# Kernel tuning notes

Measured on AMD Instinct MI355X. Metric: run time of the kernel, lower is better.

Reference implementation:

```python
import jax, jax.numpy as jnp
import numpy as np

B, S, D, H, HID = 64, 1024, 128, 4, 512
HD = D // H  # head dim = 32
EPS = 1e-5


def layer_norm(x, gamma, beta):
    mu = jnp.mean(x, axis=-1, keepdims=True)
    var = jnp.mean(jnp.square(x - mu), axis=-1, keepdims=True)
    return (x - mu) * jax.lax.rsqrt(var + EPS) * gamma + beta


def setup_inputs() -> dict:
    key = jax.random.key(0)
    ks = jax.random.split(key, 16)
    w = lambda k, shp: (jax.random.normal(k, shp, dtype=jnp.float32) * 0.02)
    return {
        "seq": jax.random.normal(ks[0], (B, S, D), dtype=jnp.float32),
        "mask": jnp.ones((B, S, 1), dtype=jnp.float32),
        "Wq": w(ks[1], (D, D)), "bq": jnp.zeros((D,), jnp.float32),
        "Wk": w(ks[2], (D, D)), "bk": jnp.zeros((D,), jnp.float32),
        "Wv": w(ks[3], (D, D)), "bv": jnp.zeros((D,), jnp.float32),
        "g1": jnp.ones((D,), jnp.float32), "be1": jnp.zeros((D,), jnp.float32),
        "g2": jnp.ones((D,), jnp.float32), "be2": jnp.zeros((D,), jnp.float32),
        "W1": w(ks[4], (D, HID)), "bm1": jnp.zeros((HID,), jnp.float32),
        "W2": w(ks[5], (HID, D)), "bm2": jnp.zeros((D,), jnp.float32),
    }


def reference(seq, mask, Wq, bq, Wk, bk, Wv, bv, g1, be1, g2, be2, W1, bm1, W2, bm2):
    # pre-norm queries; keys/values come from the RAW seq (SASRec quirk)
    q_in = layer_norm(seq, g1, be1)           # [B,S,D]
    keys = seq

    Q = (q_in @ Wq + bq).reshape(B, S, H, HD)
    K = (keys @ Wk + bk).reshape(B, S, H, HD)
    V = (keys @ Wv + bv).reshape(B, S, H, HD)

    scores = jnp.einsum("bqhd,bkhd->bhqk", Q, K) / jnp.sqrt(jnp.float32(HD))

    # key padding mask from sign of abs-sum over feature dim
    key_mask = jnp.sign(jnp.sum(jnp.abs(keys), axis=-1))      # [B,S]
    scores = jnp.where(key_mask[:, None, None, :] == 0, -jnp.inf, scores)

    # causal mask
    causal = jnp.tril(jnp.ones((S, S), dtype=bool))
    scores = jnp.where(causal[None, None], scores, -jnp.inf)

    w = jax.nn.softmax(scores, axis=-1)
    w = jnp.nan_to_num(w, nan=0.0, posinf=0.0, neginf=0.0)

    # query padding mask (on the NORMALIZED queries)
    query_mask = jnp.sign(jnp.sum(jnp.abs(q_in), axis=-1))    # [B,S]
    w = w * query_mask[:, None, :, None]
    attentions = w                                            # [B,H,S,S]

    attn_out = jnp.einsum("bhqk,bkhd->bqhd", w, V).reshape(B, S, D)

    x = attn_out + q_in
    x = layer_norm(x, g2, be2)
    h = jax.nn.relu(x @ W1 + bm1)
    y = h @ W2 + bm2 + x
    y = y * mask
    return y, attentions
```

## Files before the change

### kernel.cpp

```cpp
#include <hip/hip_runtime.h>
#include <cstddef>
#include <cstdint>

#define BB 64
#define SS 1024
#define DDIM 128
#define NH 4
#define HDIM 32
#define HIDD 512
#define EPSF 1e-5f
#define SCALEF 0.17677669529663687f
#define LOG2E 1.4426950408889634f

typedef __attribute__((ext_vector_type(8))) short short8;
typedef __attribute__((ext_vector_type(4))) short short4_t;
typedef __attribute__((ext_vector_type(4))) float f32x4;
typedef unsigned short ushort_t;

__device__ __forceinline__ unsigned short f2bf(float f) {
  unsigned u = __builtin_bit_cast(unsigned, f);
  unsigned r = (u + 0x7FFFu + ((u >> 16) & 1u)) >> 16;
  return (unsigned short)r;
}
__device__ __forceinline__ float bf2f(ushort_t h) {
  unsigned u = ((unsigned)h) << 16;
  return __builtin_bit_cast(float, u);
}

__global__ __launch_bounds__(256) void k_cvtw(
    const float* __restrict__ Wq, const float* __restrict__ Wk,
    const float* __restrict__ Wv, const float* __restrict__ W1,
    const float* __restrict__ W2,
    ushort_t* __restrict__ WqT, ushort_t* __restrict__ WkT,
    ushort_t* __restrict__ WvT, ushort_t* __restrict__ W1T,
    ushort_t* __restrict__ W2T) {
  __shared__ float tile[32][33];
  const int bid = blockIdx.x;
  const float* src; ushort_t* dst; int K, N, t0;
  if (bid < 16)       { src = Wq; dst = WqT; K = 128; N = 128; t0 = bid; }
  else if (bid < 32)  { src = Wk; dst = WkT; K = 128; N = 128; t0 = bid - 16; }
  else if (bid < 48)  { src = Wv; dst = WvT; K = 128; N = 128; t0 = bid - 32; }
  else if (bid < 112) { src = W1; dst = W1T; K = 128; N = 512; t0 = bid - 48; }
  else                { src = W2; dst = W2T; K = 512; N = 128; t0 = bid - 112; }
  const int ntile = N >> 5;
  const int k0 = (t0 / ntile) * 32, n0 = (t0 % ntile) * 32;
  const int t = threadIdx.x;
  const int r = t >> 3, c = (t & 7) * 4;
  float4 v = *(const float4*)(src + (size_t)(k0 + r) * N + n0 + c);
  tile[r][c] = v.x; tile[r][c + 1] = v.y; tile[r][c + 2] = v.z; tile[r][c + 3] = v.w;
  __syncthreads();
  ushort4 o;
  o.x = f2bf(tile[c + 0][r]); o.y = f2bf(tile[c + 1][r]);
  o.z = f2bf(tile[c + 2][r]); o.w = f2bf(tile[c + 3][r]);
  *(ushort4*)(dst + (size_t)(n0 + r) * K + k0 + c) = o;
}

__global__ __launch_bounds__(256) void k_ln1(const float* __restrict__ seq,
    const float* __restrict__ g1, const float* __restrict__ be1,
    ushort_t* __restrict__ q_in16, ushort_t* __restrict__ seq16,
    float* __restrict__ qmask, float* __restrict__ kmask) {
  const int t = threadIdx.x;
  const int r = t >> 5, cl = (t & 31) * 4;
  const int row = blockIdx.x * 8 + r;
  const size_t base = (size_t)row * DDIM + cl;
  const f32x4 v4 = *(const f32x4*)(seq + base);
  float sum = v4[0] + v4[1] + v4[2] + v4[3];
  float asum = fabsf(v4[0]) + fabsf(v4[1]) + fabsf(v4[2]) + fabsf(v4[3]);
  #pragma unroll
  for (int o = 1; o < 32; o <<= 1) { sum += __shfl_xor(sum, o); asum += __shfl_xor(asum, o); }
  const float mean = sum * (1.f / DDIM);
  f32x4 d;
  #pragma unroll
  for (int j = 0; j < 4; ++j) d[j] = v4[j] - mean;
  float sq = d[0] * d[0] + d[1] * d[1] + d[2] * d[2] + d[3] * d[3];
  #pragma unroll
  for (int o = 1; o < 32; o <<= 1) sq += __shfl_xor(sq, o);
  const float rsq = rsqrtf(sq * (1.f / DDIM) + EPSF);
  const float4 g4 = *(const float4*)(g1 + cl);
  const float4 b4 = *(const float4*)(be1 + cl);
  float qv[4];
  qv[0] = d[0] * rsq * g4.x + b4.x; qv[1] = d[1] * rsq * g4.y + b4.y;
  qv[2] = d[2] * rsq * g4.z + b4.z; qv[3] = d[3] * rsq * g4.w + b4.w;
  short4_t q4, s4;
  #pragma unroll
  for (int j = 0; j < 4; ++j) { q4[j] = (short)f2bf(qv[j]); s4[j] = (short)f2bf(v4[j]); }
  *(short4_t*)(q_in16 + base) = q4;
  *(short4_t*)(seq16 + base) = s4;
  float aq = fabsf(qv[0]) + fabsf(qv[1]) + fabsf(qv[2]) + fabsf(qv[3]);
  #pragma unroll
  for (int o = 1; o < 32; o <<= 1) aq += __shfl_xor(aq, o);
  if ((t & 31) == 0) {
    kmask[row] = asum > 0.f ? 1.f : 0.f;
    qmask[row] = aq > 0.f ? 1.f : 0.f;
  }
}

__global__ __launch_bounds__(256) void k_qkv_mfma(
    const ushort_t* __restrict__ q_in16, const ushort_t* __restrict__ seq16,
    const ushort_t* __restrict__ WqT, const ushort_t* __restrict__ WkT,
    const ushort_t* __restrict__ WvT,
    const float* __restrict__ bq, const float* __restrict__ bk,
    const float* __restrict__ bv,
    ushort_t* __restrict__ Qo, ushort_t* __restrict__ Ko,
    ushort_t* __restrict__ Vo) {
  const int m = blockIdx.y;
  const int t = threadIdx.x, w = t >> 6, lane = t & 63;
  const int lr = lane & 15, lg = lane >> 4;
  const int row = blockIdx.x * 64 + w * 16;

  if (m == 0) {
    const float sc = SCALEF * LOG2E;
    short8 a[4];
    #pragma unroll
    for (int s = 0; s < 4; ++s)
      a[s] = *(const short8*)(q_in16 + (size_t)(row + lr) * DDIM + s * 32 + lg * 8);
    #pragma unroll
    for (int nt = 0; nt < 8; ++nt) {
      f32x4 acc = {0.f, 0.f, 0.f, 0.f};
      #pragma unroll
      for (int s = 0; s < 4; ++s) {
        short8 b = *(const short8*)(WqT + (size_t)(nt * 16 + lr) * DDIM + s * 32 + lg * 8);
        acc = __builtin_amdgcn_mfma_f32_16x16x32_bf16(b, a[s], acc, 0, 0, 0);
      }
      const int n0 = nt * 16 + lg * 4;
      const float4 bb4 = *(const float4*)(bq + n0);
      short4_t o4;
      o4[0] = (short)f2bf((acc[0] + bb4.x) * sc);
      o4[1] = (short)f2bf((acc[1] + bb4.y) * sc);
      o4[2] = (short)f2bf((acc[2] + bb4.z) * sc);
      o4[3] = (short)f2bf((acc[3] + bb4.w) * sc);
      *(short4_t*)(Qo + (size_t)(row + lr) * DDIM + n0) = o4;
    }
  } else {
    short8 a[4];
    #pragma unroll
    for (int s = 0; s < 4; ++s)
      a[s] = *(const short8*)(seq16 + (size_t)(row + lr) * DDIM + s * 32 + lg * 8);
    #pragma unroll
    for (int nt = 0; nt < 8; ++nt) {
      f32x4 accK = {0.f, 0.f, 0.f, 0.f}, accV = {0.f, 0.f, 0.f, 0.f};
      #pragma unroll
      for (int s = 0; s < 4; ++s) {
        short8 bk8 = *(const short8*)(WkT + (size_t)(nt * 16 + lr) * DDIM + s * 32 + lg * 8);
        short8 bv8 = *(const short8*)(WvT + (size_t)(nt * 16 + lr) * DDIM + s * 32 + lg * 8);
        accK = __builtin_amdgcn_mfma_f32_16x16x32_bf16(bk8, a[s], accK, 0, 0, 0);
        accV = __builtin_amdgcn_mfma_f32_16x16x32_bf16(bv8, a[s], accV, 0, 0, 0);
      }
      const int n0 = nt * 16 + lg * 4;
      const float4 bk4 = *(const float4*)(bk + n0);
      const float4 bv4 = *(const float4*)(bv + n0);
      short4_t k4, v4;
      k4[0] = (short)f2bf(accK[0] + bk4.x); v4[0] = (short)f2bf(accV[0] + bv4.x);
      k4[1] = (short)f2bf(accK[1] + bk4.y); v4[1] = (short)f2bf(accV[1] + bv4.y);
      k4[2] = (short)f2bf(accK[2] + bk4.z); v4[2] = (short)f2bf(accV[2] + bv4.z);
      k4[3] = (short)f2bf(accK[3] + bk4.w); v4[3] = (short)f2bf(accV[3] + bv4.w);
      *(short4_t*)(Ko + (size_t)(row + lr) * DDIM + n0) = k4;
      *(short4_t*)(Vo + (size_t)(row + lr) * DDIM + n0) = v4;
    }
  }
}

__global__ __launch_bounds__(256) void k_attn_mfma(
    const ushort_t* __restrict__ Q, const ushort_t* __restrict__ K,
    const ushort_t* __restrict__ V,
    const float* __restrict__ qmask, const float* __restrict__ kmask,
    float* __restrict__ attn, float* __restrict__ xo) {
  __shared__ __align__(16) ushort_t Ks[2][64 * 40];
  __shared__ __align__(16) ushort_t Vts[2][32 * 72];
  __shared__ __align__(16) ushort_t Wb[4][16 * 88];

  const int t = threadIdx.x;
  const int w = t >> 6, lane = t & 63, lr = lane & 15, lg = lane >> 4;
  const int qi = 15 - (int)blockIdx.x;
  const int q0 = qi << 6;
  const int h = blockIdx.y, b = blockIdx.z;
  const int kend = q0 + 64;
  const int nch = kend >> 6;

  const size_t bS = (size_t)b * SS;
  const ushort_t* Qh = Q + bS * DDIM + h * HDIM;
  const ushort_t* Kh = K + bS * DDIM + h * HDIM;
  const ushort_t* Vh = V + bS * DDIM + h * HDIM;
  float* attn_bh = attn + (size_t)(b * NH + h) * ((size_t)SS * SS);

  {
    const int cnt4 = (SS - kend) >> 2;
    const f32x4 z = {0.f, 0.f, 0.f, 0.f};
    for (int r = w; r < 64; r += 4) {
      float* rowp = attn_bh + (size_t)(q0 + r) * SS + kend;
      for (int c = lane; c < cnt4; c += 64)
        __builtin_nontemporal_store(z, (f32x4*)(rowp + (size_t)c * 4));
    }
  }

  const int qrow = q0 + w * 16 + lr;
  const short8 qf = *(const short8*)(Qh + (size_t)qrow * DDIM + lg * 8);

  const int skr = t >> 2, skc = (t & 3) * 8;

  float lsum = 0.f;
  {
    short8 kreg = *(const short8*)(Kh + (size_t)skr * DDIM + skc);
    *(short8*)(Ks[0] + skr * 40 + skc) = kreg;
    __syncthreads();
    for (int c = 0; c < nch; ++c) {
      const int kc = c << 6;
      const int cur = c & 1;
      if (c + 1 < nch)
        kreg = *(const short8*)(Kh + (size_t)(kc + 64 + skr) * DDIM + skc);
      short8 kf[4];
      #pragma unroll
      for (int T = 0; T < 4; ++T)
        kf[T] = *(const short8*)(Ks[cur] + (T * 16 + lr) * 40 + lg * 8);
      f32x4 acc[4];
      #pragma unroll
      for (int T = 0; T < 4; ++T)
        acc[T] = __builtin_amdgcn_mfma_f32_16x16x32_bf16(kf[T], qf,
                                                         (f32x4){0.f, 0.f, 0.f, 0.f}, 0, 0, 0);
      #pragma unroll
      for (int T = 0; T < 4; ++T) {
        const int k0 = kc + T * 16 + lg * 4;
        const float4 km4 = *(const float4*)(kmask + bS + k0);
        #pragma unroll
        for (int r = 0; r < 4; ++r) {
          const float kmv = r == 0 ? km4.x : (r == 1 ? km4.y : (r == 2 ? km4.z : km4.w));
          const bool dead = (kmv == 0.f) || (k0 + r > qrow);
          lsum += dead ? 0.f : exp2f(acc[T][r]);
        }
      }
      if (c + 1 < nch)
        *(short8*)(Ks[cur ^ 1] + skr * 40 + skc) = kreg;
      __syncthreads();
    }
  }
  float ssum = lsum;
  ssum += __shfl_xor(ssum, 16);
  ssum += __shfl_xor(ssum, 32);
  const float qm = qmask[bS + qrow];
  const float inv = (ssum > 0.f) ? qm / ssum : 0.f;

  ushort_t* myW = &Wb[w][0];
  f32x4 o0 = {0.f, 0.f, 0.f, 0.f}, o1 = {0.f, 0.f, 0.f, 0.f};

  {
    short8 kreg = *(const short8*)(Kh + (size_t)skr * DDIM + skc);
    short8 vreg = *(const short8*)(Vh + (size_t)lane * DDIM + w * 8);
    *(short8*)(Ks[0] + skr * 40 + skc) = kreg;
    #pragma unroll
    for (int j = 0; j < 8; ++j) Vts[0][(w * 8 + j) * 72 + lane] = (ushort_t)vreg[j];
    __syncthreads();
    for (int c = 0; c < nch; ++c) {
      const int kc = c << 6;
      const int cur = c & 1;
      if (c + 1 < nch) {
        kreg = *(const short8*)(Kh + (size_t)(kc + 64 + skr) * DDIM + skc);
        vreg = *(const short8*)(Vh + (size_t)(kc + 64 + lane) * DDIM + w * 8);
      }
      short8 kf[4];
      #pragma unroll
      for (int T = 0; T < 4; ++T)
        kf[T] = *(const short8*)(Ks[cur] + (T * 16 + lr) * 40 + lg * 8);
      f32x4 acc[4];
      #pragma unroll
      for (int T = 0; T < 4; ++T)
        acc[T] = __builtin_amdgcn_mfma_f32_16x16x32_bf16(kf[T], qf,
                                                         (f32x4){0.f, 0.f, 0.f, 0.f}, 0, 0, 0);
      #pragma unroll
      for (int T = 0; T < 4; ++T) {
        const int k0 = kc + T * 16 + lg * 4;
        const float4 km4 = *(const float4*)(kmask + bS + k0);
        f32x4 wv4;
        #pragma unroll
        for (int r = 0; r < 4; ++r) {
          const float kmv = r == 0 ? km4.x : (r == 1 ? km4.y : (r == 2 ? km4.z : km4.w));
          const bool dead = (kmv == 0.f) || (k0 + r > qrow);
          wv4[r] = dead ? 0.f : exp2f(acc[T][r]) * inv;
        }
        __builtin_nontemporal_store(wv4, (f32x4*)(attn_bh + (size_t)qrow * SS + k0));
        short4_t p4;
        p4[0] = (short)f2bf(wv4[0]); p4[1] = (short)f2bf(wv4[1]);
        p4[2] = (short)f2bf(wv4[2]); p4[3] = (short)f2bf(wv4[3]);
        *(short4_t*)(myW + lr * 88 + T * 16 + lg * 4) = p4;
      }
      const short8 af0 = *(const short8*)(myW + lr * 88 + lg * 8);
      const short8 af1 = *(const short8*)(myW + lr * 88 + 32 + lg * 8);
      const short8 vb00 = *(const short8*)(Vts[cur] + (size_t)(lr) * 72 + lg * 8);
      const short8 vb10 = *(const short8*)(Vts[cur] + (size_t)(lr) * 72 + 32 + lg * 8);
      const short8 vb01 = *(const short8*)(Vts[cur] + (size_t)(16 + lr) * 72 + lg * 8);
      const short8 vb11 = *(const short8*)(Vts[cur] + (size_t)(16 + lr) * 72 + 32 + lg * 8);
      o0 = __builtin_amdgcn_mfma_f32_16x16x32_bf16(vb00, af0, o0, 0, 0, 0);
      o0 = __builtin_amdgcn_mfma_f32_16x16x32_bf16(vb10, af1, o0, 0, 0, 0);
      o1 = __builtin_amdgcn_mfma_f32_16x16x32_bf16(vb01, af0, o1, 0, 0, 0);
      o1 = __builtin_amdgcn_mfma_f32_16x16x32_bf16(vb11, af1, o1, 0, 0, 0);
      if (c + 1 < nch) {
        *(short8*)(Ks[cur ^ 1] + skr * 40 + skc) = kreg;
        #pragma unroll
        for (int j = 0; j < 8; ++j) Vts[cur ^ 1][(w * 8 + j) * 72 + lane] = (ushort_t)vreg[j];
      }
      __syncthreads();
    }
  }

  {
    float* op = xo + (bS + qrow) * DDIM + h * HDIM;
    *(f32x4*)(op + lg * 4) = o0;
    *(f32x4*)(op + 16 + lg * 4) = o1;
  }
}

__global__ __launch_bounds__(256) void k_mlp_fused(
    const float* __restrict__ xo, const ushort_t* __restrict__ q_in16,
    const float* __restrict__ g2, const float* __restrict__ be2,
    const ushort_t* __restrict__ W1T, const float* __restrict__ bm1,
    const ushort_t* __restrict__ W2T, const float* __restrict__ bm2,
    const float* __restrict__ mask, float* __restrict__ y) {
  __shared__ __align__(16) ushort_t xls[64 * 136];
  __shared__ __align__(16) ushort_t hs[4][16 * 140];
  const int t = threadIdx.x, w = t >> 6, lane = t & 63;
  const int lr = lane & 15, lg = lane >> 4;
  const int row0 = blockIdx.x * 64;

  {
    const int r = t >> 2, s = t & 3;
    const size_t base = (size_t)(row0 + r) * DDIM + s * 32;
    float v[32];
    float sum = 0.f, sq = 0.f;
    #pragma unroll
    for (int i = 0; i < 4; ++i) {
      const f32x4 x4a = *(const f32x4*)(xo + base + i * 8);
      const f32x4 x4b = *(const f32x4*)(xo + base + i * 8 + 4);
      const short8 q8 = *(const short8*)(q_in16 + base + i * 8);
      #pragma unroll
      for (int j = 0; j < 4; ++j) {
        v[i * 8 + j] = x4a[j] + bf2f((ushort_t)q8[j]);
        v[i * 8 + 4 + j] = x4b[j] + bf2f((ushort_t)q8[4 + j]);
      }
    }
    #pragma unroll
    for (int i = 0; i < 32; ++i) { sum += v[i]; sq += v[i] * v[i]; }
    sum += __shfl_xor(sum, 1); sum += __shfl_xor(sum, 2);
    sq  += __shfl_xor(sq, 1);  sq  += __shfl_xor(sq, 2);
    const float mean = sum * (1.f / DDIM);
    const float var = sq * (1.f / DDIM) - mean * mean;
    const float rsq = rsqrtf(var + EPSF);
    #pragma unroll
    for (int i = 0; i < 8; ++i) {
      const f32x4 g4 = *(const f32x4*)(g2 + s * 32 + i * 4);
      const f32x4 b4 = *(const f32x4*)(be2 + s * 32 + i * 4);
      short4_t o4;
      #pragma unroll
      for (int j = 0; j < 4; ++j)
        o4[j] = (short)f2bf((v[i * 4 + j] - mean) * rsq * g4[j] + b4[j]);
      *(short4_t*)(xls + r * 136 + s * 32 + i * 4) = o4;
    }
  }
  __syncthreads();

  ushort_t* myh = &hs[w][0];
  short8 xa[4];
  #pragma unroll
  for (int s = 0; s < 4; ++s)
    xa[s] = *(const short8*)(xls + (w * 16 + lr) * 136 + s * 32 + lg * 8);

  f32x4 yacc[8];
  #pragma unroll
  for (int i = 0; i < 8; ++i) yacc[i] = (f32x4){0.f, 0.f, 0.f, 0.f};

  for (int c = 0; c < 4; ++c) {
    #pragma unroll
    for (int nt = 0; nt < 8; ++nt) {
      f32x4 acc = {0.f, 0.f, 0.f, 0.f};
      #pragma unroll
      for (int s = 0; s < 4; ++s) {
        short8 b = *(const short8*)(W1T + (size_t)(c * 128 + nt * 16 + lr) * DDIM + s * 32 + lg * 8);
        acc = __builtin_amdgcn_mfma_f32_16x16x32_bf16(b, xa[s], acc, 0, 0, 0);
      }
      const int n0 = nt * 16 + lg * 4;
      const float4 bb4 = *(const float4*)(bm1 + c * 128 + n0);
      short4_t hp;
      hp[0] = (short)f2bf(fmaxf(acc[0] + bb4.x, 0.f));
      hp[1] = (short)f2bf(fmaxf(acc[1] + bb4.y, 0.f));
      hp[2] = (short)f2bf(fmaxf(acc[2] + bb4.z, 0.f));
      hp[3] = (short)f2bf(fmaxf(acc[3] + bb4.w, 0.f));
      *(short4_t*)(myh + lr * 140 + n0) = hp;
    }
    short8 a2[4];
    #pragma unroll
    for (int s = 0; s < 4; ++s)
      a2[s] = *(const short8*)(myh + lr * 140 + s * 32 + lg * 8);
    #pragma unroll
    for (int nt = 0; nt < 8; ++nt) {
      #pragma unroll
      for (int s = 0; s < 4; ++s) {
        short8 b = *(const short8*)(W2T + (size_t)(nt * 16 + lr) * HIDD + c * 128 + s * 32 + lg * 8);
        yacc[nt] = __builtin_amdgcn_mfma_f32_16x16x32_bf16(b, a2[s], yacc[nt], 0, 0, 0);
      }
    }
  }

  const int rr = row0 + w * 16 + lr;
  const float mk = mask[rr];
  #pragma unroll
  for (int nt = 0; nt < 8; ++nt) {
    const int n0 = nt * 16 + lg * 4;
    const float4 bb4 = *(const float4*)(bm2 + n0);
    const ushort4 xv = *(const ushort4*)(xls + (w * 16 + lr) * 136 + n0);
    f32x4 out;
    out[0] = (yacc[nt][0] + bb4.x + bf2f(xv.x)) * mk;
    out[1] = (yacc[nt][1] + bb4.y + bf2f(xv.y)) * mk;
    out[2] = (yacc[nt][2] + bb4.z + bf2f(xv.z)) * mk;
    out[3] = (yacc[nt][3] + bb4.w + bf2f(xv.w)) * mk;
    *(f32x4*)(y + (size_t)rr * DDIM + n0) = out;
  }
}

extern "C" void kernel_launch(void* const* d_in, const int* in_sizes, int n_in,
                              void* d_out, int out_size, void* d_ws, size_t ws_size,
                              hipStream_t stream) {
  const float* seq  = (const float*)d_in[0];
  const float* mask = (const float*)d_in[1];
  const float* Wq = (const float*)d_in[2];
  const float* bq = (const float*)d_in[3];
  const float* Wk = (const float*)d_in[4];
  const float* bk = (const float*)d_in[5];
  const float* Wv = (const float*)d_in[6];
  const float* bv = (const float*)d_in[7];
  const float* g1 = (const float*)d_in[8];
  const float* be1 = (const float*)d_in[9];
  const float* g2 = (const float*)d_in[10];
  const float* be2 = (const float*)d_in[11];
  const float* W1 = (const float*)d_in[12];
  const float* bm1 = (const float*)d_in[13];
  const float* W2 = (const float*)d_in[14];
  const float* bm2 = (const float*)d_in[15];

  float* ws   = (float*)d_ws;
  float* xb   = ws;
  float* qmk  = ws + 8388608;
  float* kmk  = ws + 8454144;
  ushort_t* sbase  = (ushort_t*)(ws + 8519680);
  ushort_t* Qb     = sbase;
  ushort_t* Kb     = sbase + 8388608;
  ushort_t* Vb     = sbase + 16777216;
  ushort_t* q_in16 = sbase + 25165824;
  ushort_t* seq16  = sbase + 33554432;
  ushort_t* WqT    = sbase + 41943040;
  ushort_t* WkT    = WqT + 16384;
  ushort_t* WvT    = WkT + 16384;
  ushort_t* W1T    = WvT + 16384;
  ushort_t* W2T    = W1T + 65536;

  float* y    = (float*)d_out;
  float* attn = y + 8388608;

  hipLaunchKernelGGL(k_cvtw, dim3(176), dim3(256), 0, stream,
                     Wq, Wk, Wv, W1, W2, WqT, WkT, WvT, W1T, W2T);
  hipLaunchKernelGGL(k_ln1, dim3(BB * SS / 8), dim3(256), 0, stream,
                     seq, g1, be1, q_in16, seq16, qmk, kmk);
  hipLaunchKernelGGL(k_qkv_mfma, dim3(1024, 2), dim3(256), 0, stream,
                     q_in16, seq16, WqT, WkT, WvT, bq, bk, bv, Qb, Kb, Vb);
  hipLaunchKernelGGL(k_attn_mfma, dim3(16, NH, BB), dim3(256), 0, stream,
                     Qb, Kb, Vb, qmk, kmk, attn, xb);
  hipLaunchKernelGGL(k_mlp_fused, dim3(1024), dim3(256), 0, stream,
                     xb, q_in16, g2, be2, W1T, bm1, W2T, bm2, mask, y);
}
```

Measured before the change: 573.7 us.

## Fuse LayerNorm into QKV projection and give attention blocks 128 query rows

```diff
diff --git a/kernel.cpp b/kernel.cpp
--- a/kernel.cpp
+++ b/kernel.cpp
@@ -55,112 +55,120 @@
   *(ushort4*)(dst + (size_t)(n0 + r) * K + k0 + c) = o;
 }
 
-__global__ __launch_bounds__(256) void k_ln1(const float* __restrict__ seq,
+__global__ __launch_bounds__(256) void k_ln1_qkv(
+    const float* __restrict__ seq,
     const float* __restrict__ g1, const float* __restrict__ be1,
-    ushort_t* __restrict__ q_in16, ushort_t* __restrict__ seq16,
-    float* __restrict__ qmask, float* __restrict__ kmask) {
-  const int t = threadIdx.x;
-  const int r = t >> 5, cl = (t & 31) * 4;
-  const int row = blockIdx.x * 8 + r;
-  const size_t base = (size_t)row * DDIM + cl;
-  const f32x4 v4 = *(const f32x4*)(seq + base);
-  float sum = v4[0] + v4[1] + v4[2] + v4[3];
-  float asum = fabsf(v4[0]) + fabsf(v4[1]) + fabsf(v4[2]) + fabsf(v4[3]);
-  #pragma unroll
-  for (int o = 1; o < 32; o <<= 1) { sum += __shfl_xor(sum, o); asum += __shfl_xor(asum, o); }
-  const float mean = sum * (1.f / DDIM);
-  f32x4 d;
-  #pragma unroll
-  for (int j = 0; j < 4; ++j) d[j] = v4[j] - mean;
-  float sq = d[0] * d[0] + d[1] * d[1] + d[2] * d[2] + d[3] * d[3];
-  #pragma unroll
-  for (int o = 1; o < 32; o <<= 1) sq += __shfl_xor(sq, o);
-  const float rsq = rsqrtf(sq * (1.f / DDIM) + EPSF);
-  const float4 g4 = *(const float4*)(g1 + cl);
-  const float4 b4 = *(const float4*)(be1 + cl);
-  float qv[4];
-  qv[0] = d[0] * rsq * g4.x + b4.x; qv[1] = d[1] * rsq * g4.y + b4.y;
-  qv[2] = d[2] * rsq * g4.z + b4.z; qv[3] = d[3] * rsq * g4.w + b4.w;
-  short4_t q4, s4;
-  #pragma unroll
-  for (int j = 0; j < 4; ++j) { q4[j] = (short)f2bf(qv[j]); s4[j] = (short)f2bf(v4[j]); }
-  *(short4_t*)(q_in16 + base) = q4;
-  *(short4_t*)(seq16 + base) = s4;
-  float aq = fabsf(qv[0]) + fabsf(qv[1]) + fabsf(qv[2]) + fabsf(qv[3]);
-  #pragma unroll
-  for (int o = 1; o < 32; o <<= 1) aq += __shfl_xor(aq, o);
-  if ((t & 31) == 0) {
-    kmask[row] = asum > 0.f ? 1.f : 0.f;
-    qmask[row] = aq > 0.f ? 1.f : 0.f;
-  }
-}
-
-__global__ __launch_bounds__(256) void k_qkv_mfma(
-    const ushort_t* __restrict__ q_in16, const ushort_t* __restrict__ seq16,
     const ushort_t* __restrict__ WqT, const ushort_t* __restrict__ WkT,
     const ushort_t* __restrict__ WvT,
     const float* __restrict__ bq, const float* __restrict__ bk,
     const float* __restrict__ bv,
+    ushort_t* __restrict__ q_in16,
     ushort_t* __restrict__ Qo, ushort_t* __restrict__ Ko,
-    ushort_t* __restrict__ Vo) {
-  const int m = blockIdx.y;
-  const int t = threadIdx.x, w = t >> 6, lane = t & 63;
+    ushort_t* __restrict__ Vo,
+    float* __restrict__ qmask, float* __restrict__ kmask) {
+  __shared__ __align__(16) ushort_t qls[64 * 136];
+  __shared__ __align__(16) ushort_t sls[64 * 136];
+  const int t = threadIdx.x;
+  const int row0 = blockIdx.x * 64;
+
+  {
+    const int r = t >> 2, s = t & 3;
+    const size_t base = (size_t)(row0 + r) * DDIM + s * 32;
+    float v[32];
+    float sum = 0.f, asum = 0.f;
+    #pragma unroll
+    for (int i = 0; i < 8; ++i) {
+      const f32x4 x4 = *(const f32x4*)(seq + base + i * 4);
+      #pragma unroll
+      for (int j = 0; j < 4; ++j) {
+        v[i * 4 + j] = x4[j];
+        sum += x4[j]; asum += fabsf(x4[j]);
+      }
+    }
+    sum += __shfl_xor(sum, 1); sum += __shfl_xor(sum, 2);
+    asum += __shfl_xor(asum, 1); asum += __shfl_xor(asum, 2);
+    const float mean = sum * (1.f / DDIM);
+    float sq = 0.f;
+    #pragma unroll
+    for (int i = 0; i < 32; ++i) { const float d = v[i] - mean; sq += d * d; }
+    sq += __shfl_xor(sq, 1); sq += __shfl_xor(sq, 2);
+    const float rsq = rsqrtf(sq * (1.f / DDIM) + EPSF);
+    float aq = 0.f;
+    #pragma unroll
+    for (int i = 0; i < 8; ++i) {
+      const f32x4 g4 = *(const f32x4*)(g1 + s * 32 + i * 4);
+      const f32x4 b4 = *(const f32x4*)(be1 + s * 32 + i * 4);
+      short4_t q4, s4v;
+      #pragma unroll
+      for (int j = 0; j < 4; ++j) {
+        const float qv = (v[i * 4 + j] - mean) * rsq * g4[j] + b4[j];
+        aq += fabsf(qv);
+        q4[j] = (short)f2bf(qv);
+        s4v[j] = (short)f2bf(v[i * 4 + j]);
+      }
+      *(short4_t*)(qls + r * 136 + s * 32 + i * 4) = q4;
+      *(short4_t*)(sls + r * 136 + s * 32 + i * 4) = s4v;
+      *(short4_t*)(q_in16 + base + i * 4) = q4;
+    }
+    aq += __shfl_xor(aq, 1); aq += __shfl_xor(aq, 2);
+    if (s == 0) {
+      kmask[row0 + r] = asum > 0.f ? 1.f : 0.f;
+      qmask[row0 + r] = aq > 0.f ? 1.f : 0.f;
+    }
+  }
+  __syncthreads();
+
+  const int w = t >> 6, lane = t & 63;
   const int lr = lane & 15, lg = lane >> 4;
-  const int row = blockIdx.x * 64 + w * 16;
-
-  if (m == 0) {
-    const float sc = SCALEF * LOG2E;
-    short8 a[4];
-    #pragma unroll
-    for (int s = 0; s < 4; ++s)
-      a[s] = *(const short8*)(q_in16 + (size_t)(row + lr) * DDIM + s * 32 + lg * 8);
-    #pragma unroll
-    for (int nt = 0; nt < 8; ++nt) {
-      f32x4 acc = {0.f, 0.f, 0.f, 0.f};
-      #pragma unroll
-      for (int s = 0; s < 4; ++s) {
-        short8 b = *(const short8*)(WqT + (size_t)(nt * 16 + lr) * DDIM + s * 32 + lg * 8);
-        acc = __builtin_amdgcn_mfma_f32_16x16x32_bf16(b, a[s], acc, 0, 0, 0);
-      }
-      const int n0 = nt * 16 + lg * 4;
-      const float4 bb4 = *(const float4*)(bq + n0);
-      short4_t o4;
-      o4[0] = (short)f2bf((acc[0] + bb4.x) * sc);
-      o4[1] = (short)f2bf((acc[1] + bb4.y) * sc);
-      o4[2] = (short)f2bf((acc[2] + bb4.z) * sc);
-      o4[3] = (short)f2bf((acc[3] + bb4.w) * sc);
-      *(short4_t*)(Qo + (size_t)(row + lr) * DDIM + n0) = o4;
-    }
-  } else {
-    short8 a[4];
-    #pragma unroll
-    for (int s = 0; s < 4; ++s)
-      a[s] = *(const short8*)(seq16 + (size_t)(row + lr) * DDIM + s * 32 + lg * 8);
-    #pragma unroll
-    for (int nt = 0; nt < 8; ++nt) {
-      f32x4 accK = {0.f, 0.f, 0.f, 0.f}, accV = {0.f, 0.f, 0.f, 0.f};
-      #pragma unroll
-      for (int s = 0; s < 4; ++s) {
-        short8 bk8 = *(const short8*)(WkT + (size_t)(nt * 16 + lr) * DDIM + s * 32 + lg * 8);
-        short8 bv8 = *(const short8*)(WvT + (size_t)(nt * 16 + lr) * DDIM + s * 32 + lg * 8);
-        accK = __builtin_amdgcn_mfma_f32_16x16x32_bf16(bk8, a[s], accK, 0, 0, 0);
-        accV = __builtin_amdgcn_mfma_f32_16x16x32_bf16(bv8, a[s], accV, 0, 0, 0);
-      }
-      const int n0 = nt * 16 + lg * 4;
-      const float4 bk4 = *(const float4*)(bk + n0);
-      const float4 bv4 = *(const float4*)(bv + n0);
-      short4_t k4, v4;
-      k4[0] = (short)f2bf(accK[0] + bk4.x); v4[0] = (short)f2bf(accV[0] + bv4.x);
-      k4[1] = (short)f2bf(accK[1] + bk4.y); v4[1] = (short)f2bf(accV[1] + bv4.y);
-      k4[2] = (short)f2bf(accK[2] + bk4.z); v4[2] = (short)f2bf(accV[2] + bv4.z);
-      k4[3] = (short)f2bf(accK[3] + bk4.w); v4[3] = (short)f2bf(accV[3] + bv4.w);
-      *(short4_t*)(Ko + (size_t)(row + lr) * DDIM + n0) = k4;
-      *(short4_t*)(Vo + (size_t)(row + lr) * DDIM + n0) = v4;
-    }
-  }
-}
-
-__global__ __launch_bounds__(256) void k_attn_mfma(
+  const int rloc = w * 16 + lr;
+  short8 qa[4], sa[4];
+  #pragma unroll
+  for (int s4 = 0; s4 < 4; ++s4) {
+    qa[s4] = *(const short8*)(qls + rloc * 136 + s4 * 32 + lg * 8);
+    sa[s4] = *(const short8*)(sls + rloc * 136 + s4 * 32 + lg * 8);
+  }
+  const float qsc = SCALEF * LOG2E;
+  #pragma unroll
+  for (int nt = 0; nt < 8; ++nt) {
+    f32x4 acc = {0.f, 0.f, 0.f, 0.f};
+    #pragma unroll
+    for (int s4 = 0; s4 < 4; ++s4) {
+      short8 b = *(const short8*)(WqT + (size_t)(nt * 16 + lr) * DDIM + s4 * 32 + lg * 8);
+      acc = __builtin_amdgcn_mfma_f32_16x16x32_bf16(b, qa[s4], acc, 0, 0, 0);
+    }
+    const int n0 = nt * 16 + lg * 4;
+    const float4 bb4 = *(const float4*)(bq + n0);
+    short4_t o4;
+    o4[0] = (short)f2bf((acc[0] + bb4.x) * qsc);
+    o4[1] = (short)f2bf((acc[1] + bb4.y) * qsc);
+    o4[2] = (short)f2bf((acc[2] + bb4.z) * qsc);
+    o4[3] = (short)f2bf((acc[3] + bb4.w) * qsc);
+    *(short4_t*)(Qo + (size_t)(row0 + rloc) * DDIM + n0) = o4;
+  }
+  #pragma unroll
+  for (int nt = 0; nt < 8; ++nt) {
+    f32x4 accK = {0.f, 0.f, 0.f, 0.f}, accV = {0.f, 0.f, 0.f, 0.f};
+    #pragma unroll
+    for (int s4 = 0; s4 < 4; ++s4) {
+      short8 bk8 = *(const short8*)(WkT + (size_t)(nt * 16 + lr) * DDIM + s4 * 32 + lg * 8);
+      short8 bv8 = *(const short8*)(WvT + (size_t)(nt * 16 + lr) * DDIM + s4 * 32 + lg * 8);
+      accK = __builtin_amdgcn_mfma_f32_16x16x32_bf16(bk8, sa[s4], accK, 0, 0, 0);
+      accV = __builtin_amdgcn_mfma_f32_16x16x32_bf16(bv8, sa[s4], accV, 0, 0, 0);
+    }
+    const int n0 = nt * 16 + lg * 4;
+    const float4 bk4 = *(const float4*)(bk + n0);
+    const float4 bv4 = *(const float4*)(bv + n0);
+    short4_t k4, v4;
+    k4[0] = (short)f2bf(accK[0] + bk4.x); v4[0] = (short)f2bf(accV[0] + bv4.x);
+    k4[1] = (short)f2bf(accK[1] + bk4.y); v4[1] = (short)f2bf(accV[1] + bv4.y);
+    k4[2] = (short)f2bf(accK[2] + bk4.z); v4[2] = (short)f2bf(accV[2] + bv4.z);
+    k4[3] = (short)f2bf(accK[3] + bk4.w); v4[3] = (short)f2bf(accV[3] + bv4.w);
+    *(short4_t*)(Ko + (size_t)(row0 + rloc) * DDIM + n0) = k4;
+    *(short4_t*)(Vo + (size_t)(row0 + rloc) * DDIM + n0) = v4;
+  }
+}
+
+__global__ __launch_bounds__(256, 4) void k_attn_mfma(
     const ushort_t* __restrict__ Q, const ushort_t* __restrict__ K,
     const ushort_t* __restrict__ V,
     const float* __restrict__ qmask, const float* __restrict__ kmask,
@@ -171,10 +179,10 @@
 
   const int t = threadIdx.x;
   const int w = t >> 6, lane = t & 63, lr = lane & 15, lg = lane >> 4;
-  const int qi = 15 - (int)blockIdx.x;
-  const int q0 = qi << 6;
+  const int qi = 7 - (int)blockIdx.x;
+  const int q0 = qi << 7;
   const int h = blockIdx.y, b = blockIdx.z;
-  const int kend = q0 + 64;
+  const int kend = q0 + 128;
   const int nch = kend >> 6;
 
   const size_t bS = (size_t)b * SS;
@@ -186,19 +194,22 @@
   {
     const int cnt4 = (SS - kend) >> 2;
     const f32x4 z = {0.f, 0.f, 0.f, 0.f};
-    for (int r = w; r < 64; r += 4) {
+    for (int r = w; r < 128; r += 4) {
       float* rowp = attn_bh + (size_t)(q0 + r) * SS + kend;
       for (int c = lane; c < cnt4; c += 64)
         __builtin_nontemporal_store(z, (f32x4*)(rowp + (size_t)c * 4));
     }
   }
 
-  const int qrow = q0 + w * 16 + lr;
-  const short8 qf = *(const short8*)(Qh + (size_t)qrow * DDIM + lg * 8);
+  const int qrow0 = q0 + w * 16 + lr;
+  const int qrow1 = qrow0 + 64;
+  const int deadlim = q0 + w * 16 + 15;
+  const short8 qf0 = *(const short8*)(Qh + (size_t)qrow0 * DDIM + lg * 8);
+  const short8 qf1 = *(const short8*)(Qh + (size_t)qrow1 * DDIM + lg * 8);
 
   const int skr = t >> 2, skc = (t & 3) * 8;
 
-  float lsum = 0.f;
+  float lsum0 = 0.f, lsum1 = 0.f;
   {
     short8 kreg = *(const short8*)(Kh + (size_t)skr * DDIM + skc);
     *(short8*)(Ks[0] + skr * 40 + skc) = kreg;
@@ -212,20 +223,42 @@
       #pragma unroll
       for (int T = 0; T < 4; ++T)
         kf[T] = *(const short8*)(Ks[cur] + (T * 16 + lr) * 40 + lg * 8);
-      f32x4 acc[4];
+      float4 km4[4];
       #pragma unroll
       for (int T = 0; T < 4; ++T)
-        acc[T] = __builtin_amdgcn_mfma_f32_16x16x32_bf16(kf[T], qf,
-                                                         (f32x4){0.f, 0.f, 0.f, 0.f}, 0, 0, 0);
-      #pragma unroll
-      for (int T = 0; T < 4; ++T) {
-        const int k0 = kc + T * 16 + lg * 4;
-        const float4 km4 = *(const float4*)(kmask + bS + k0);
-        #pragma unroll
-        for (int r = 0; r < 4; ++r) {
-          const float kmv = r == 0 ? km4.x : (r == 1 ? km4.y : (r == 2 ? km4.z : km4.w));
-          const bool dead = (kmv == 0.f) || (k0 + r > qrow);
-          lsum += dead ? 0.f : exp2f(acc[T][r]);
+        km4[T] = *(const float4*)(kmask + bS + kc + T * 16 + lg * 4);
+      if (kc <= deadlim) {
+        f32x4 acc0[4];
+        #pragma unroll
+        for (int T = 0; T < 4; ++T)
+          acc0[T] = __builtin_amdgcn_mfma_f32_16x16x32_bf16(kf[T], qf0,
+                                                            (f32x4){0.f, 0.f, 0.f, 0.f}, 0, 0, 0);
+        #pragma unroll
+        for (int T = 0; T < 4; ++T) {
+          const int k0 = kc + T * 16 + lg * 4;
+          #pragma unroll
+          for (int r = 0; r < 4; ++r) {
+            const float kmv = r == 0 ? km4[T].x : (r == 1 ? km4[T].y : (r == 2 ? km4[T].z : km4[T].w));
+            const bool dead = (kmv == 0.f) || (k0 + r > qrow0);
+            lsum0 += dead ? 0.f : exp2f(acc0[T][r]);
+          }
+        }
+      }
+      {
+        f32x4 acc1[4];
+        #pragma unroll
+        for (int T = 0; T < 4; ++T)
+          acc1[T] = __builtin_amdgcn_mfma_f32_16x16x32_bf16(kf[T], qf1,
+                                                            (f32x4){0.f, 0.f, 0.f, 0.f}, 0, 0, 0);
+        #pragma unroll
+        for (int T = 0; T < 4; ++T) {
+          const int k0 = kc + T * 16 + lg * 4;
+          #pragma unroll
+          for (int r = 0; r < 4; ++r) {
+            const float kmv = r == 0 ? km4[T].x : (r == 1 ? km4[T].y : (r == 2 ? km4[T].z : km4[T].w));
+            const bool dead = (kmv == 0.f) || (k0 + r > qrow1);
+            lsum1 += dead ? 0.f : exp2f(acc1[T][r]);
+          }
         }
       }
       if (c + 1 < nch)
@@ -233,14 +266,15 @@
       __syncthreads();
     }
   }
-  float ssum = lsum;
-  ssum += __shfl_xor(ssum, 16);
-  ssum += __shfl_xor(ssum, 32);
-  const float qm = qmask[bS + qrow];
-  const float inv = (ssum > 0.f) ? qm / ssum : 0.f;
+  float ssum0 = lsum0, ssum1 = lsum1;
+  ssum0 += __shfl_xor(ssum0, 16); ssum0 += __shfl_xor(ssum0, 32);
+  ssum1 += __shfl_xor(ssum1, 16); ssum1 += __shfl_xor(ssum1, 32);
+  const float inv0 = (ssum0 > 0.f) ? qmask[bS + qrow0] / ssum0 : 0.f;
+  const float inv1 = (ssum1 > 0.f) ? qmask[bS + qrow1] / ssum1 : 0.f;
 
   ushort_t* myW = &Wb[w][0];
   f32x4 o0 = {0.f, 0.f, 0.f, 0.f}, o1 = {0.f, 0.f, 0.f, 0.f};
+  f32x4 o2 = {0.f, 0.f, 0.f, 0.f}, o3 = {0.f, 0.f, 0.f, 0.f};
 
   {
     short8 kreg = *(const short8*)(Kh + (size_t)skr * DDIM + skc);
@@ -260,38 +294,84 @@
       #pragma unroll
       for (int T = 0; T < 4; ++T)
         kf[T] = *(const short8*)(Ks[cur] + (T * 16 + lr) * 40 + lg * 8);
-      f32x4 acc[4];
+      float4 km4[4];
       #pragma unroll
       for (int T = 0; T < 4; ++T)
-        acc[T] = __builtin_amdgcn_mfma_f32_16x16x32_bf16(kf[T], qf,
-                                                         (f32x4){0.f, 0.f, 0.f, 0.f}, 0, 0, 0);
-      #pragma unroll
-      for (int T = 0; T < 4; ++T) {
-        const int k0 = kc + T * 16 + lg * 4;
-        const float4 km4 = *(const float4*)(kmask + bS + k0);
-        f32x4 wv4;
-        #pragma unroll
-        for (int r = 0; r < 4; ++r) {
-          const float kmv = r == 0 ? km4.x : (r == 1 ? km4.y : (r == 2 ? km4.z : km4.w));
-          const bool dead = (kmv == 0.f) || (k0 + r > qrow);
-          wv4[r] = dead ? 0.f : exp2f(acc[T][r]) * inv;
+        km4[T] = *(const float4*)(kmask + bS + kc + T * 16 + lg * 4);
+
+      if (kc <= deadlim) {
+        f32x4 acc0[4];
+        #pragma unroll
+        for (int T = 0; T < 4; ++T)
+          acc0[T] = __builtin_amdgcn_mfma_f32_16x16x32_bf16(kf[T], qf0,
+                                                            (f32x4){0.f, 0.f, 0.f, 0.f}, 0, 0, 0);
+        #pragma unroll
+        for (int T = 0; T < 4; ++T) {
+          const int k0 = kc + T * 16 + lg * 4;
+          f32x4 wv4;
+          #pragma unroll
+          for (int r = 0; r < 4; ++r) {
+            const float kmv = r == 0 ? km4[T].x : (r == 1 ? km4[T].y : (r == 2 ? km4[T].z : km4[T].w));
+            const bool dead = (kmv == 0.f) || (k0 + r > qrow0);
+            wv4[r] = dead ? 0.f : exp2f(acc0[T][r]) * inv0;
+          }
+          __builtin_nontemporal_store(wv4, (f32x4*)(attn_bh + (size_t)qrow0 * SS + k0));
+          short4_t p4;
+          p4[0] = (short)f2bf(wv4[0]); p4[1] = (short)f2bf(wv4[1]);
+          p4[2] = (short)f2bf(wv4[2]); p4[3] = (short)f2bf(wv4[3]);
+          *(short4_t*)(myW + lr * 88 + T * 16 + lg * 4) = p4;
         }
-        __builtin_nontemporal_store(wv4, (f32x4*)(attn_bh + (size_t)qrow * SS + k0));
-        short4_t p4;
-        p4[0] = (short)f2bf(wv4[0]); p4[1] = (short)f2bf(wv4[1]);
-        p4[2] = (short)f2bf(wv4[2]); p4[3] = (short)f2bf(wv4[3]);
-        *(short4_t*)(myW + lr * 88 + T * 16 + lg * 4) = p4;
-      }
-      const short8 af0 = *(const short8*)(myW + lr * 88 + lg * 8);
-      const short8 af1 = *(const short8*)(myW + lr * 88 + 32 + lg * 8);
-      const short8 vb00 = *(const short8*)(Vts[cur] + (size_t)(lr) * 72 + lg * 8);
-      const short8 vb10 = *(const short8*)(Vts[cur] + (size_t)(lr) * 72 + 32 + lg * 8);
-      const short8 vb01 = *(const short8*)(Vts[cur] + (size_t)(16 + lr) * 72 + lg * 8);
-      const short8 vb11 = *(const short8*)(Vts[cur] + (size_t)(16 + lr) * 72 + 32 + lg * 8);
-      o0 = __builtin_amdgcn_mfma_f32_16x16x32_bf16(vb00, af0, o0, 0, 0, 0);
-      o0 = __builtin_amdgcn_mfma_f32_16x16x32_bf16(vb10, af1, o0, 0, 0, 0);
-      o1 = __builtin_amdgcn_mfma_f32_16x16x32_bf16(vb01, af0, o1, 0, 0, 0);
-      o1 = __builtin_amdgcn_mfma_f32_16x16x32_bf16(vb11, af1, o1, 0, 0, 0);
+        const short8 af0 = *(const short8*)(myW + lr * 88 + lg * 8);
+        const short8 af1 = *(const short8*)(myW + lr * 88 + 32 + lg * 8);
+        const short8 vb00 = *(const short8*)(Vts[cur] + (size_t)(lr) * 72 + lg * 8);
+        const short8 vb10 = *(const short8*)(Vts[cur] + (size_t)(lr) * 72 + 32 + lg * 8);
+        const short8 vb01 = *(const short8*)(Vts[cur] + (size_t)(16 + lr) * 72 + lg * 8);
+        const short8 vb11 = *(const short8*)(Vts[cur] + (size_t)(16 + lr) * 72 + 32 + lg * 8);
+        o0 = __builtin_amdgcn_mfma_f32_16x16x32_bf16(vb00, af0, o0, 0, 0, 0);
+        o0 = __builtin_amdgcn_mfma_f32_16x16x32_bf16(vb10, af1, o0, 0, 0, 0);
+        o1 = __builtin_amdgcn_mfma_f32_16x16x32_bf16(vb01, af0, o1, 0, 0, 0);
+        o1 = __builtin_amdgcn_mfma_f32_16x16x32_bf16(vb11, af1, o1, 0, 0, 0);
+      } else {
+        const f32x4 z = {0.f, 0.f, 0.f, 0.f};
+        #pragma unroll
+        for (int T = 0; T < 4; ++T)
+          __builtin_nontemporal_store(z, (f32x4*)(attn_bh + (size_t)qrow0 * SS + kc + T * 16 + lg * 4));
+      }
+
+      {
+        f32x4 acc1[4];
+        #pragma unroll
+        for (int T = 0; T < 4; ++T)
+          acc1[T] = __builtin_amdgcn_mfma_f32_16x16x32_bf16(kf[T], qf1,
+                                                            (f32x4){0.f, 0.f, 0.f, 0.f}, 0, 0, 0);
+        #pragma unroll
+        for (int T = 0; T < 4; ++T) {
+          const int k0 = kc + T * 16 + lg * 4;
+          f32x4 wv4;
+          #pragma unroll
+          for (int r = 0; r < 4; ++r) {
+            const float kmv = r == 0 ? km4[T].x : (r == 1 ? km4[T].y : (r == 2 ? km4[T].z : km4[T].w));
+            const bool dead = (kmv == 0.f) || (k0 + r > qrow1);
+            wv4[r] = dead ? 0.f : exp2f(acc1[T][r]) * inv1;
+          }
+          __builtin_nontemporal_store(wv4, (f32x4*)(attn_bh + (size_t)qrow1 * SS + k0));
+          short4_t p4;
+          p4[0] = (short)f2bf(wv4[0]); p4[1] = (short)f2bf(wv4[1]);
+          p4[2] = (short)f2bf(wv4[2]); p4[3] = (short)f2bf(wv4[3]);
+          *(short4_t*)(myW + lr * 88 + T * 16 + lg * 4) = p4;
+        }
+        const short8 af0 = *(const short8*)(myW + lr * 88 + lg * 8);
+        const short8 af1 = *(const short8*)(myW + lr * 88 + 32 + lg * 8);
+        const short8 vb00 = *(const short8*)(Vts[cur] + (size_t)(lr) * 72 + lg * 8);
+        const short8 vb10 = *(const short8*)(Vts[cur] + (size_t)(lr) * 72 + 32 + lg * 8);
+        const short8 vb01 = *(const short8*)(Vts[cur] + (size_t)(16 + lr) * 72 + lg * 8);
+        const short8 vb11 = *(const short8*)(Vts[cur] + (size_t)(16 + lr) * 72 + 32 + lg * 8);
+        o2 = __builtin_amdgcn_mfma_f32_16x16x32_bf16(vb00, af0, o2, 0, 0, 0);
+        o2 = __builtin_amdgcn_mfma_f32_16x16x32_bf16(vb10, af1, o2, 0, 0, 0);
+        o3 = __builtin_amdgcn_mfma_f32_16x16x32_bf16(vb01, af0, o3, 0, 0, 0);
+        o3 = __builtin_amdgcn_mfma_f32_16x16x32_bf16(vb11, af1, o3, 0, 0, 0);
+      }
+
       if (c + 1 < nch) {
         *(short8*)(Ks[cur ^ 1] + skr * 40 + skc) = kreg;
         #pragma unroll
@@ -302,9 +382,12 @@
   }
 
   {
-    float* op = xo + (bS + qrow) * DDIM + h * HDIM;
-    *(f32x4*)(op + lg * 4) = o0;
-    *(f32x4*)(op + 16 + lg * 4) = o1;
+    float* op0 = xo + (bS + qrow0) * DDIM + h * HDIM;
+    *(f32x4*)(op0 + lg * 4) = o0;
+    *(f32x4*)(op0 + 16 + lg * 4) = o1;
+    float* op1 = xo + (bS + qrow1) * DDIM + h * HDIM;
+    *(f32x4*)(op1 + lg * 4) = o2;
+    *(f32x4*)(op1 + 16 + lg * 4) = o3;
   }
 }
 
@@ -443,8 +526,7 @@
   ushort_t* Kb     = sbase + 8388608;
   ushort_t* Vb     = sbase + 16777216;
   ushort_t* q_in16 = sbase + 25165824;
-  ushort_t* seq16  = sbase + 33554432;
-  ushort_t* WqT    = sbase + 41943040;
+  ushort_t* WqT    = sbase + 33554432;
   ushort_t* WkT    = WqT + 16384;
   ushort_t* WvT    = WkT + 16384;
   ushort_t* W1T    = WvT + 16384;
@@ -455,11 +537,10 @@
 
   hipLaunchKernelGGL(k_cvtw, dim3(176), dim3(256), 0, stream,
                      Wq, Wk, Wv, W1, W2, WqT, WkT, WvT, W1T, W2T);
-  hipLaunchKernelGGL(k_ln1, dim3(BB * SS / 8), dim3(256), 0, stream,
-                     seq, g1, be1, q_in16, seq16, qmk, kmk);
-  hipLaunchKernelGGL(k_qkv_mfma, dim3(1024, 2), dim3(256), 0, stream,
-                     q_in16, seq16, WqT, WkT, WvT, bq, bk, bv, Qb, Kb, Vb);
-  hipLaunchKernelGGL(k_attn_mfma, dim3(16, NH, BB), dim3(256), 0, stream,
+  hipLaunchKernelGGL(k_ln1_qkv, dim3(1024), dim3(256), 0, stream,
+                     seq, g1, be1, WqT, WkT, WvT, bq, bk, bv,
+                     q_in16, Qb, Kb, Vb, qmk, kmk);
+  hipLaunchKernelGGL(k_attn_mfma, dim3(8, NH, BB), dim3(256), 0, stream,
                      Qb, Kb, Vb, qmk, kmk, attn, xb);
   hipLaunchKernelGGL(k_mlp_fused, dim3(1024), dim3(256), 0, stream,
                      xb, q_in16, g2, be2, W1T, bm1, W2T, bm2, mask, y);
```

Result: slower. 610.6 us (+6.4%).

## Load whole-head K and V into LDS once per block, loop query tiles per wave

Applied to the files above, without the earlier changes.

```diff
diff --git a/kernel.cpp b/kernel.cpp
--- a/kernel.cpp
+++ b/kernel.cpp
@@ -160,22 +160,20 @@
   }
 }
 
-__global__ __launch_bounds__(256) void k_attn_mfma(
+#define KST 36
+#define VST 1032
+__global__ __launch_bounds__(512, 2) void k_attn_mfma(
     const ushort_t* __restrict__ Q, const ushort_t* __restrict__ K,
     const ushort_t* __restrict__ V,
     const float* __restrict__ qmask, const float* __restrict__ kmask,
     float* __restrict__ attn, float* __restrict__ xo) {
-  __shared__ __align__(16) ushort_t Ks[2][64 * 40];
-  __shared__ __align__(16) ushort_t Vts[2][32 * 72];
-  __shared__ __align__(16) ushort_t Wb[4][16 * 88];
+  __shared__ __align__(16) ushort_t Ks[1024 * KST];
+  __shared__ __align__(16) ushort_t Vts[32 * VST];
+  __shared__ __align__(16) ushort_t Wb[8][16 * 72];
 
   const int t = threadIdx.x;
   const int w = t >> 6, lane = t & 63, lr = lane & 15, lg = lane >> 4;
-  const int qi = 15 - (int)blockIdx.x;
-  const int q0 = qi << 6;
-  const int h = blockIdx.y, b = blockIdx.z;
-  const int kend = q0 + 64;
-  const int nch = kend >> 6;
+  const int h = blockIdx.x, b = blockIdx.y;
 
   const size_t bS = (size_t)b * SS;
   const ushort_t* Qh = Q + bS * DDIM + h * HDIM;
@@ -184,34 +182,55 @@
   float* attn_bh = attn + (size_t)(b * NH + h) * ((size_t)SS * SS);
 
   {
-    const int cnt4 = (SS - kend) >> 2;
-    const f32x4 z = {0.f, 0.f, 0.f, 0.f};
-    for (int r = w; r < 64; r += 4) {
-      float* rowp = attn_bh + (size_t)(q0 + r) * SS + kend;
-      for (int c = lane; c < cnt4; c += 64)
-        __builtin_nontemporal_store(z, (f32x4*)(rowp + (size_t)c * 4));
-    }
-  }
-
-  const int qrow = q0 + w * 16 + lr;
-  const short8 qf = *(const short8*)(Qh + (size_t)qrow * DDIM + lg * 8);
-
-  const int skr = t >> 2, skc = (t & 3) * 8;
-
-  float lsum = 0.f;
+    const int r0 = t >> 2, sc = (t & 3) * 8;
+    #pragma unroll
+    for (int i = 0; i < 8; ++i) {
+      const int r = r0 + i * 128;
+      const short8 kv = *(const short8*)(Kh + (size_t)r * DDIM + sc);
+      *(short4_t*)(Ks + r * KST + sc) = *(const short4_t*)&kv;
+      *(short4_t*)(Ks + r * KST + sc + 4) = *((const short4_t*)&kv + 1);
+    }
+  }
   {
-    short8 kreg = *(const short8*)(Kh + (size_t)skr * DDIM + skc);
-    *(short8*)(Ks[0] + skr * 40 + skc) = kreg;
-    __syncthreads();
+    #pragma unroll
+    for (int c = 0; c < 16; ++c) {
+      const int k = c * 64 + lane;
+      const short4_t v4 = *(const short4_t*)(Vh + (size_t)k * DDIM + w * 4);
+      #pragma unroll
+      for (int j = 0; j < 4; ++j)
+        Vts[(w * 4 + j) * VST + k] = (ushort_t)v4[j];
+    }
+  }
+  __syncthreads();
+
+  ushort_t* myW = &Wb[w][0];
+
+  #pragma unroll 1
+  for (int i = 0; i < 8; ++i) {
+    const int st = w + 8 * i;
+    const int qrow = st * 16 + lr;
+    const int nch = (st >> 2) + 1;
+    const int kend = nch << 6;
+
+    {
+      const f32x4 z = {0.f, 0.f, 0.f, 0.f};
+      float* rowp = attn_bh + (size_t)qrow * SS;
+      for (int k4 = kend + lg * 4; k4 < SS; k4 += 16)
+        __builtin_nontemporal_store(z, (f32x4*)(rowp + k4));
+    }
+
+    const short8 qf = *(const short8*)(Qh + (size_t)qrow * DDIM + lg * 8);
+
+    float lsum = 0.f;
     for (int c = 0; c < nch; ++c) {
       const int kc = c << 6;
-      const int cur = c & 1;
-      if (c + 1 < nch)
-        kreg = *(const short8*)(Kh + (size_t)(kc + 64 + skr) * DDIM + skc);
       short8 kf[4];
       #pragma unroll
-      for (int T = 0; T < 4; ++T)
-        kf[T] = *(const short8*)(Ks[cur] + (T * 16 + lr) * 40 + lg * 8);
+      for (int T = 0; T < 4; ++T) {
+        const ushort_t* kp = Ks + (kc + T * 16 + lr) * KST + lg * 8;
+        *(short4_t*)&kf[T] = *(const short4_t*)kp;
+        *((short4_t*)&kf[T] + 1) = *(const short4_t*)(kp + 4);
+      }
       f32x4 acc[4];
       #pragma unroll
       for (int T = 0; T < 4; ++T)
@@ -228,38 +247,22 @@
           lsum += dead ? 0.f : exp2f(acc[T][r]);
         }
       }
-      if (c + 1 < nch)
-        *(short8*)(Ks[cur ^ 1] + skr * 40 + skc) = kreg;
-      __syncthreads();
-    }
-  }
-  float ssum = lsum;
-  ssum += __shfl_xor(ssum, 16);
-  ssum += __shfl_xor(ssum, 32);
-  const float qm = qmask[bS + qrow];
-  const float inv = (ssum > 0.f) ? qm / ssum : 0.f;
-
-  ushort_t* myW = &Wb[w][0];
-  f32x4 o0 = {0.f, 0.f, 0.f, 0.f}, o1 = {0.f, 0.f, 0.f, 0.f};
-
-  {
-    short8 kreg = *(const short8*)(Kh + (size_t)skr * DDIM + skc);
-    short8 vreg = *(const short8*)(Vh + (size_t)lane * DDIM + w * 8);
-    *(short8*)(Ks[0] + skr * 40 + skc) = kreg;
-    #pragma unroll
-    for (int j = 0; j < 8; ++j) Vts[0][(w * 8 + j) * 72 + lane] = (ushort_t)vreg[j];
-    __syncthreads();
+    }
+    float ssum = lsum;
+    ssum += __shfl_xor(ssum, 16);
+    ssum += __shfl_xor(ssum, 32);
+    const float inv = (ssum > 0.f) ? qmask[bS + qrow] / ssum : 0.f;
+
+    f32x4 o0 = {0.f, 0.f, 0.f, 0.f}, o1 = {0.f, 0.f, 0.f, 0.f};
     for (int c = 0; c < nch; ++c) {
       const int kc = c << 6;
-      const int cur = c & 1;
-      if (c + 1 < nch) {
-        kreg = *(const short8*)(Kh + (size_t)(kc + 64 + skr) * DDIM + skc);
-        vreg = *(const short8*)(Vh + (size_t)(kc + 64 + lane) * DDIM + w * 8);
-      }
       short8 kf[4];
       #pragma unroll
-      for (int T = 0; T < 4; ++T)
-        kf[T] = *(const short8*)(Ks[cur] + (T * 16 + lr) * 40 + lg * 8);
+      for (int T = 0; T < 4; ++T) {
+        const ushort_t* kp = Ks + (kc + T * 16 + lr) * KST + lg * 8;
+        *(short4_t*)&kf[T] = *(const short4_t*)kp;
+        *((short4_t*)&kf[T] + 1) = *(const short4_t*)(kp + 4);
+      }
       f32x4 acc[4];
       #pragma unroll
       for (int T = 0; T < 4; ++T)
@@ -280,28 +283,20 @@
         short4_t p4;
         p4[0] = (short)f2bf(wv4[0]); p4[1] = (short)f2bf(wv4[1]);
         p4[2] = (short)f2bf(wv4[2]); p4[3] = (short)f2bf(wv4[3]);
-        *(short4_t*)(myW + lr * 88 + T * 16 + lg * 4) = p4;
-      }
-      const short8 af0 = *(const short8*)(myW + lr * 88 + lg * 8);
-      const short8 af1 = *(const short8*)(myW + lr * 88 + 32 + lg * 8);
-      const short8 vb00 = *(const short8*)(Vts[cur] + (size_t)(lr) * 72 + lg * 8);
-      const short8 vb10 = *(const short8*)(Vts[cur] + (size_t)(lr) * 72 + 32 + lg * 8);
-      const short8 vb01 = *(const short8*)(Vts[cur] + (size_t)(16 + lr) * 72 + lg * 8);
-      const short8 vb11 = *(const short8*)(Vts[cur] + (size_t)(16 + lr) * 72 + 32 + lg * 8);
+        *(short4_t*)(myW + lr * 72 + T * 16 + lg * 4) = p4;
+      }
+      const short8 af0 = *(const short8*)(myW + lr * 72 + lg * 8);
+      const short8 af1 = *(const short8*)(myW + lr * 72 + 32 + lg * 8);
+      const short8 vb00 = *(const short8*)(Vts + (size_t)(lr) * VST + kc + lg * 8);
+      const short8 vb10 = *(const short8*)(Vts + (size_t)(lr) * VST + kc + 32 + lg * 8);
+      const short8 vb01 = *(const short8*)(Vts + (size_t)(16 + lr) * VST + kc + lg * 8);
+      const short8 vb11 = *(const short8*)(Vts + (size_t)(16 + lr) * VST + kc + 32 + lg * 8);
       o0 = __builtin_amdgcn_mfma_f32_16x16x32_bf16(vb00, af0, o0, 0, 0, 0);
       o0 = __builtin_amdgcn_mfma_f32_16x16x32_bf16(vb10, af1, o0, 0, 0, 0);
       o1 = __builtin_amdgcn_mfma_f32_16x16x32_bf16(vb01, af0, o1, 0, 0, 0);
       o1 = __builtin_amdgcn_mfma_f32_16x16x32_bf16(vb11, af1, o1, 0, 0, 0);
-      if (c + 1 < nch) {
-        *(short8*)(Ks[cur ^ 1] + skr * 40 + skc) = kreg;
-        #pragma unroll
-        for (int j = 0; j < 8; ++j) Vts[cur ^ 1][(w * 8 + j) * 72 + lane] = (ushort_t)vreg[j];
-      }
-      __syncthreads();
-    }
-  }
-
-  {
+    }
+
     float* op = xo + (bS + qrow) * DDIM + h * HDIM;
     *(f32x4*)(op + lg * 4) = o0;
     *(f32x4*)(op + 16 + lg * 4) = o1;
@@ -459,7 +454,7 @@
                      seq, g1, be1, q_in16, seq16, qmk, kmk);
   hipLaunchKernelGGL(k_qkv_mfma, dim3(1024, 2), dim3(256), 0, stream,
                      q_in16, seq16, WqT, WkT, WvT, bq, bk, bv, Qb, Kb, Vb);
-  hipLaunchKernelGGL(k_attn_mfma, dim3(16, NH, BB), dim3(256), 0, stream,
+  hipLaunchKernelGGL(k_attn_mfma, dim3(NH, BB), dim3(512), 0, stream,
                      Qb, Kb, Vb, qmk, kmk, attn, xb);
   hipLaunchKernelGGL(k_mlp_fused, dim3(1024), dim3(256), 0, stream,
                      xb, q_in16, g2, be2, W1T, bm1, W2T, bm2, mask, y);
```

Result: slower. 587.9 us (+2.5%).
